# Optimization experiments

Measured on AMD Instinct MI355X. Metric: run time of the kernel, lower is better.

## Reference

```python
import jax, jax.numpy as jnp
import numpy as np

B, D, U = 4096, 256, 512


def setup_inputs() -> dict:
    key = jax.random.key(0)
    k = jax.random.split(key, 7)
    return {
        "x": jax.random.normal(k[0], (B, D), jnp.float32),
        "t": jax.random.uniform(k[1], (B, 1), jnp.float32),           # elapsed-time input
        "h0": jax.random.normal(k[2], (B, U), jnp.float32),
        "c0": jax.random.normal(k[3], (B, U), jnp.float32),
        "kernel": jax.random.normal(k[4], (D, 5 * U), jnp.float32) / np.sqrt(D).astype(np.float32),
        "recurrent_kernel": jax.random.normal(k[5], (U, 3 * U), jnp.float32) / np.sqrt(U).astype(np.float32),
        "kernel_time": jax.random.normal(k[6], (1, 3 * U), jnp.float32) * 0.1,
    }


def reference(x, t, h0, c0, kernel, recurrent_kernel, kernel_time):
    sig = jax.nn.sigmoid
    # Fused input projection: one GEMM instead of 5 (same math, kernel cols are
    # ordered [i, c, o, t1, t2] exactly as the original slices self.kernel).
    x_i, x_c, x_o, x_t1, x_t2 = jnp.split(x @ kernel, 5, axis=1)          # each (B, U)
    # Fused recurrent projection: cols ordered [i, c, o].
    r_i, r_c, r_o = jnp.split(h0 @ recurrent_kernel, 3, axis=1)           # each (B, U)
    # Time projections: cols ordered [t1, t2, o].
    kt1, kt2, kto = jnp.split(t @ kernel_time, 3, axis=1)                 # each (B, U)

    i = sig(x_i + r_i)
    t_1 = sig(x_t1 + sig(kt1))
    # tf.where(t_1 > -1e-5, -1e-5, t_1): sigmoid output is always > -1e-5,
    # so this clamps to the constant -1e-5; keep the where for faithfulness.
    NEG_EPS = jnp.float32(-1e-5)
    t_1_constraint = jnp.where(t_1 > NEG_EPS, jnp.full_like(t_1, NEG_EPS), t_1)
    t_2 = sig(x_t2 + sig(kt2))
    c_tilde = jnp.tanh(x_c + r_c)
    c_m_ = (1.0 - i * t_1) * c0 + i * c_tilde * t_1_constraint
    c_m = (1.0 - i) * c0 + i * c_tilde * t_2
    o = sig(x_o + r_o + kto)
    h = jnp.tanh(c_m_) * o
    # original returns (h, [h, c_m]); h appears twice, so return (h, c_m)
    return (h, c_m)
```

## Files before the change

### kernel.cpp

```cpp
#include <hip/hip_runtime.h>


typedef __attribute__((ext_vector_type(8))) short short8_t;
typedef __attribute__((ext_vector_type(4))) float f32x4_t;
typedef unsigned int u32;

#define B_N 4096
#define D_K 256
#define U_N 512

__device__ __forceinline__ unsigned short f2bf(float f) {
    unsigned int x = __float_as_uint(f);
    unsigned int r = x + 0x7fffu + ((x >> 16) & 1u);
    return (unsigned short)(r >> 16);
}

__device__ __forceinline__ float sigf(float z) {
    return 1.0f / (1.0f + __expf(-z));
}

__device__ __forceinline__ float tanhfast(float z) {
    return 1.0f - 2.0f / (1.0f + __expf(2.0f * z));
}

__device__ __forceinline__ void gl16(const unsigned short* g, unsigned short* l) {
    __builtin_amdgcn_global_load_lds(
        (const __attribute__((address_space(1))) u32*)g,
        (__attribute__((address_space(3))) u32*)l, 16, 0, 0);
}

#define SWZ(r, kc) ((((r) * 8) + ((kc) ^ ((r) & 7))) * 8)

__global__ __launch_bounds__(256) void prep(
    const float* __restrict__ x, const float* __restrict__ h0,
    const float* __restrict__ kern, const float* __restrict__ rk,
    unsigned short* __restrict__ xs, unsigned short* __restrict__ hs,
    unsigned short* __restrict__ ksw, unsigned short* __restrict__ rsw)
{
    const int c = blockIdx.x * 256 + threadIdx.x;
    if (c < 131072) {
        const int t = c >> 10, q = c & 1023;
        const int row = q >> 3, kc = q & 7;
        const int rb = t >> 2, kb = t & 3;
        const float* s = x + (size_t)(rb * 128 + row) * D_K + kb * 64 + kc * 8;
        short8_t o;
#pragma unroll
        for (int j = 0; j < 8; ++j) o[j] = (short)f2bf(s[j]);
        *reinterpret_cast<short8_t*>(xs + (size_t)t * 8192 + SWZ(row, kc)) = o;
    } else if (c < 393216) {
        const int c2 = c - 131072;
        const int t = c2 >> 10, q = c2 & 1023;
        const int row = q >> 3, kc = q & 7;
        const int rb = t >> 3, kb = t & 7;
        const float* s = h0 + (size_t)(rb * 128 + row) * U_N + kb * 64 + kc * 8;
        short8_t o;
#pragma unroll
        for (int j = 0; j < 8; ++j) o[j] = (short)f2bf(s[j]);
        *reinterpret_cast<short8_t*>(hs + (size_t)t * 8192 + SWZ(row, kc)) = o;
    } else if (c < 475136) {
        const int c2 = c - 393216;
        const int t = c2 / 1280, q = c2 - t * 1280;
        const int kc = q / 160, r = q - kc * 160;
        const int nb = t >> 2, kb = t & 3;
        const int col = (r >> 5) * U_N + nb * 32 + (r & 31);
        short8_t o;
#pragma unroll
        for (int j = 0; j < 8; ++j)
            o[j] = (short)f2bf(kern[(size_t)(kb * 64 + kc * 8 + j) * 2560 + col]);
        *reinterpret_cast<short8_t*>(ksw + (size_t)t * 10240 + SWZ(r, kc)) = o;
    } else {
        const int c2 = c - 475136;
        const int t = c2 / 768, q = c2 - t * 768;
        const int kc = q / 96, r = q - kc * 96;
        const int nb = t >> 3, kb = t & 7;
        const int col = (r >> 5) * U_N + nb * 32 + (r & 31);
        short8_t o;
#pragma unroll
        for (int j = 0; j < 8; ++j)
            o[j] = (short)f2bf(rk[(size_t)(kb * 64 + kc * 8 + j) * 1536 + col]);
        *reinterpret_cast<short8_t*>(rsw + (size_t)t * 6144 + SWZ(r, kc)) = o;
    }
}

__global__ __launch_bounds__(256, 2) void tlstm_main(
    const unsigned short* __restrict__ xs,
    const unsigned short* __restrict__ hs,
    const unsigned short* __restrict__ ksw,
    const unsigned short* __restrict__ rsw,
    const float* __restrict__ tvec,
    const float* __restrict__ c0,
    const float* __restrict__ ktime,
    float* __restrict__ out)
{
    __shared__ __align__(16) unsigned short lds[2][18432];

    const int tid = threadIdx.x;
    const int wave = tid >> 6;
    const int lane = tid & 63;
    const int lr = lane & 15;
    const int lq = lane >> 4;
    const int wm = wave >> 1;
    const int wn = wave & 1;
    const int nb = blockIdx.x;
    const int rb = blockIdx.y;

    f32x4_t acc[8][4];
#pragma unroll
    for (int m = 0; m < 8; ++m)
#pragma unroll
        for (int p = 0; p < 4; ++p)
            acc[m][p] = (f32x4_t){0.f, 0.f, 0.f, 0.f};

    auto stage = [&](int s, int buf) {
        unsigned short* ab = &lds[buf][0];
        unsigned short* bb = &lds[buf][8192];
        if (s < 4) {
            const unsigned short* at = xs + (size_t)(rb * 4 + s) * 8192;
#pragma unroll
            for (int j = 0; j < 4; ++j)
                gl16(at + (j * 256 + tid) * 8, ab + (j * 256 + wave * 64) * 8);
            const unsigned short* bt = ksw + (size_t)(nb * 4 + s) * 10240;
#pragma unroll
            for (int j = 0; j < 5; ++j)
                gl16(bt + (j * 256 + tid) * 8, bb + (j * 256 + wave * 64) * 8);
        } else {
            const unsigned short* at = hs + (size_t)(rb * 8 + (s - 4)) * 8192;
#pragma unroll
            for (int j = 0; j < 4; ++j)
                gl16(at + (j * 256 + tid) * 8, ab + (j * 256 + wave * 64) * 8);
            const unsigned short* bt = rsw + (size_t)(nb * 8 + (s - 4)) * 6144;
#pragma unroll
            for (int j = 0; j < 3; ++j)
                gl16(bt + (j * 256 + tid) * 8, bb + (j * 256 + wave * 64) * 8);
        }
    };

    auto compute1 = [&](int buf) {
        const unsigned short* ab = &lds[buf][0];
        const unsigned short* bb = &lds[buf][8192];
#pragma unroll
        for (int ks = 0; ks < 2; ++ks) {
            const int kc = ks * 4 + lq;
            short8_t a[4];
#pragma unroll
            for (int p = 0; p < 4; ++p)
                a[p] = *reinterpret_cast<const short8_t*>(ab + SWZ(wm * 64 + p * 16 + lr, kc));
#pragma unroll
            for (int m = 0; m < 5; ++m) {
                const int r = m * 32 + wn * 16 + lr;
                short8_t b = *reinterpret_cast<const short8_t*>(bb + SWZ(r, kc));
#pragma unroll
                for (int p = 0; p < 4; ++p)
                    acc[m][p] = __builtin_amdgcn_mfma_f32_16x16x32_bf16(a[p], b, acc[m][p], 0, 0, 0);
            }
        }
    };

    auto compute2 = [&](int buf) {
        const unsigned short* ab = &lds[buf][0];
        const unsigned short* bb = &lds[buf][8192];
#pragma unroll
        for (int ks = 0; ks < 2; ++ks) {
            const int kc = ks * 4 + lq;
            short8_t a[4];
#pragma unroll
            for (int p = 0; p < 4; ++p)
                a[p] = *reinterpret_cast<const short8_t*>(ab + SWZ(wm * 64 + p * 16 + lr, kc));
#pragma unroll
            for (int m = 0; m < 3; ++m) {
                const int r = m * 32 + wn * 16 + lr;
                short8_t b = *reinterpret_cast<const short8_t*>(bb + SWZ(r, kc));
#pragma unroll
                for (int p = 0; p < 4; ++p)
                    acc[5 + m][p] = __builtin_amdgcn_mfma_f32_16x16x32_bf16(a[p], b, acc[5 + m][p], 0, 0, 0);
            }
        }
    };

    int cur = 0;
    stage(0, 0);
    __syncthreads();
#pragma unroll 1
    for (int s = 0; s < 12; ++s) {
        if (s < 11) stage(s + 1, cur ^ 1);
        if (s < 4) compute1(cur); else compute2(cur);
        __syncthreads();
        cur ^= 1;
    }

    const float NEG_EPS = -1e-5f;
    const int u = nb * 32 + wn * 16 + lr;
    const float kt1 = ktime[u];
    const float kt2 = ktime[U_N + u];
    const float kto = ktime[2 * U_N + u];
#pragma unroll
    for (int p = 0; p < 4; ++p)
#pragma unroll
        for (int i2 = 0; i2 < 4; ++i2) {
            const int b = rb * 128 + wm * 64 + p * 16 + lq * 4 + i2;
            const float tb = tvec[b];
            const float c0v = c0[(size_t)b * U_N + u];
            const float x_i  = acc[0][p][i2];
            const float x_c  = acc[1][p][i2];
            const float x_o  = acc[2][p][i2];
            const float x_t1 = acc[3][p][i2];
            const float x_t2 = acc[4][p][i2];
            const float r_i  = acc[5][p][i2];
            const float r_c  = acc[6][p][i2];
            const float r_o  = acc[7][p][i2];

            const float ig  = sigf(x_i + r_i);
            const float t1v = sigf(x_t1 + sigf(tb * kt1));
            const float t1c = (t1v > NEG_EPS) ? NEG_EPS : t1v;
            const float t2v = sigf(x_t2 + sigf(tb * kt2));
            const float ct  = tanhfast(x_c + r_c);
            const float cm_ = (1.f - ig * t1v) * c0v + ig * ct * t1c;
            const float cm  = (1.f - ig) * c0v + ig * ct * t2v;
            const float og  = sigf(x_o + r_o + tb * kto);

            out[(size_t)b * U_N + u] = tanhfast(cm_) * og;
            out[(size_t)B_N * U_N + (size_t)b * U_N + u] = cm;
        }

}

extern "C" void kernel_launch(void* const* d_in, const int* in_sizes, int n_in,
                              void* d_out, int out_size, void* d_ws, size_t ws_size,
                              hipStream_t stream) {
    const float* x     = (const float*)d_in[0];
    const float* t     = (const float*)d_in[1];
    const float* h0    = (const float*)d_in[2];
    const float* c0    = (const float*)d_in[3];
    const float* kern  = (const float*)d_in[4];
    const float* rk    = (const float*)d_in[5];
    const float* ktime = (const float*)d_in[6];
    float* out = (float*)d_out;

    unsigned short* xs  = (unsigned short*)d_ws;
    unsigned short* hs  = (unsigned short*)((char*)d_ws + 2097152);
    unsigned short* ksw = (unsigned short*)((char*)d_ws + 6291456);
    unsigned short* rsw = (unsigned short*)((char*)d_ws + 7602176);

    prep<<<2240, 256, 0, stream>>>(x, h0, kern, rk, xs, hs, ksw, rsw);
    tlstm_main<<<dim3(16, 32), 256, 0, stream>>>(
        xs, hs, ksw, rsw, t, c0, ktime, out);
}
```

Baseline: 33.19 us.

## Widen main tile to 64 units with 512 threads and unrolled vmcnt pipeline

Each block now covers 64 hidden units with 8 waves and 512 threads instead of 32 units with 4 waves, so every A tile loaded into LDS serves twice as many columns and the grid halves. The K loop is fully unrolled with explicit s_waitcnt vmcnt and raw barriers in place of __syncthreads, so the next stage's loads can stay in flight while the current stage computes. The c0 values are prefetched into registers during the last stages, hiding their latency before the epilogue. The costs are more LDS per block (about 112 KB for the two buffers), which limits occupancy, and hand-counted vmcnt values that must exactly match the number of loads issued per stage.

```diff
diff --git a/kernel.cpp b/kernel.cpp
--- a/kernel.cpp
+++ b/kernel.cpp
@@ -30,6 +30,10 @@
 }
 
 #define SWZ(r, kc) ((((r) * 8) + ((kc) ^ ((r) & 7))) * 8)
+
+#define WAIT_VM(N)                                            \
+    asm volatile("s_waitcnt vmcnt(" #N ")" ::: "memory");     \
+    __builtin_amdgcn_sched_barrier(0)
 
 __global__ __launch_bounds__(256) void prep(
     const float* __restrict__ x, const float* __restrict__ h0,
@@ -82,7 +86,7 @@
     }
 }
 
-__global__ __launch_bounds__(256, 2) void tlstm_main(
+__global__ __launch_bounds__(512, 2) void tlstm_main(
     const unsigned short* __restrict__ xs,
     const unsigned short* __restrict__ hs,
     const unsigned short* __restrict__ ksw,
@@ -92,46 +96,58 @@
     const float* __restrict__ ktime,
     float* __restrict__ out)
 {
-    __shared__ __align__(16) unsigned short lds[2][18432];
+    __shared__ __align__(16) unsigned short lds[2][28672];
 
     const int tid = threadIdx.x;
     const int wave = tid >> 6;
     const int lane = tid & 63;
     const int lr = lane & 15;
     const int lq = lane >> 4;
-    const int wm = wave >> 1;
-    const int wn = wave & 1;
+    const int wm = wave >> 2;
+    const int wn = wave & 3;
     const int nb = blockIdx.x;
     const int rb = blockIdx.y;
 
+    const int u = nb * 64 + wn * 16 + lr;
+
     f32x4_t acc[8][4];
 #pragma unroll
     for (int m = 0; m < 8; ++m)
 #pragma unroll
         for (int p = 0; p < 4; ++p)
             acc[m][p] = (f32x4_t){0.f, 0.f, 0.f, 0.f};
+
+    float c0r[16];
 
     auto stage = [&](int s, int buf) {
         unsigned short* ab = &lds[buf][0];
         unsigned short* bb = &lds[buf][8192];
         if (s < 4) {
             const unsigned short* at = xs + (size_t)(rb * 4 + s) * 8192;
-#pragma unroll
-            for (int j = 0; j < 4; ++j)
-                gl16(at + (j * 256 + tid) * 8, ab + (j * 256 + wave * 64) * 8);
-            const unsigned short* bt = ksw + (size_t)(nb * 4 + s) * 10240;
-#pragma unroll
-            for (int j = 0; j < 5; ++j)
-                gl16(bt + (j * 256 + tid) * 8, bb + (j * 256 + wave * 64) * 8);
+            gl16(at + (size_t)tid * 8,         ab + (size_t)(wave * 64) * 8);
+            gl16(at + (size_t)(512 + tid) * 8, ab + (size_t)(512 + wave * 64) * 8);
+            const unsigned short* b0 = ksw + (size_t)(nb * 8 + s) * 10240;
+            const unsigned short* b1 = ksw + (size_t)(nb * 8 + 4 + s) * 10240;
+#pragma unroll
+            for (int j = 0; j < 5; ++j) {
+                const int c = j * 512 + tid;
+                const unsigned short* src = (c < 1280) ? (b0 + (size_t)c * 8)
+                                                       : (b1 + (size_t)(c - 1280) * 8);
+                gl16(src, bb + (size_t)(j * 512 + wave * 64) * 8);
+            }
         } else {
             const unsigned short* at = hs + (size_t)(rb * 8 + (s - 4)) * 8192;
-#pragma unroll
-            for (int j = 0; j < 4; ++j)
-                gl16(at + (j * 256 + tid) * 8, ab + (j * 256 + wave * 64) * 8);
-            const unsigned short* bt = rsw + (size_t)(nb * 8 + (s - 4)) * 6144;
-#pragma unroll
-            for (int j = 0; j < 3; ++j)
-                gl16(bt + (j * 256 + tid) * 8, bb + (j * 256 + wave * 64) * 8);
+            gl16(at + (size_t)tid * 8,         ab + (size_t)(wave * 64) * 8);
+            gl16(at + (size_t)(512 + tid) * 8, ab + (size_t)(512 + wave * 64) * 8);
+            const unsigned short* b0 = rsw + (size_t)(nb * 16 + (s - 4)) * 6144;
+            const unsigned short* b1 = rsw + (size_t)(nb * 16 + 8 + (s - 4)) * 6144;
+#pragma unroll
+            for (int j = 0; j < 3; ++j) {
+                const int c = j * 512 + tid;
+                const unsigned short* src = (c < 768) ? (b0 + (size_t)c * 8)
+                                                      : (b1 + (size_t)(c - 768) * 8);
+                gl16(src, bb + (size_t)(j * 512 + wave * 64) * 8);
+            }
         }
     };
 
@@ -147,7 +163,7 @@
                 a[p] = *reinterpret_cast<const short8_t*>(ab + SWZ(wm * 64 + p * 16 + lr, kc));
 #pragma unroll
             for (int m = 0; m < 5; ++m) {
-                const int r = m * 32 + wn * 16 + lr;
+                const int r = (wn >> 1) * 160 + m * 32 + (wn & 1) * 16 + lr;
                 short8_t b = *reinterpret_cast<const short8_t*>(bb + SWZ(r, kc));
 #pragma unroll
                 for (int p = 0; p < 4; ++p)
@@ -168,7 +184,7 @@
                 a[p] = *reinterpret_cast<const short8_t*>(ab + SWZ(wm * 64 + p * 16 + lr, kc));
 #pragma unroll
             for (int m = 0; m < 3; ++m) {
-                const int r = m * 32 + wn * 16 + lr;
+                const int r = (wn >> 1) * 96 + m * 32 + (wn & 1) * 16 + lr;
                 short8_t b = *reinterpret_cast<const short8_t*>(bb + SWZ(r, kc));
 #pragma unroll
                 for (int p = 0; p < 4; ++p)
@@ -177,19 +193,41 @@
         }
     };
 
-    int cur = 0;
+#define K_BODY(S, NV, CF)                                  \
+    {                                                      \
+        WAIT_VM(NV);                                       \
+        __builtin_amdgcn_s_barrier();                      \
+        __builtin_amdgcn_sched_barrier(0);                 \
+        CF((S) & 1);                                       \
+        __builtin_amdgcn_sched_barrier(0);                 \
+        __builtin_amdgcn_s_barrier();                      \
+        __builtin_amdgcn_sched_barrier(0);                 \
+    }
+
     stage(0, 0);
-    __syncthreads();
-#pragma unroll 1
-    for (int s = 0; s < 12; ++s) {
-        if (s < 11) stage(s + 1, cur ^ 1);
-        if (s < 4) compute1(cur); else compute2(cur);
-        __syncthreads();
-        cur ^= 1;
-    }
+    stage(1, 1);  K_BODY(0, 7,  compute1);
+    stage(2, 0);  K_BODY(1, 7,  compute1);
+    stage(3, 1);  K_BODY(2, 7,  compute1);
+    stage(4, 0);  K_BODY(3, 5,  compute1);
+    stage(5, 1);  K_BODY(4, 5,  compute2);
+    stage(6, 0);  K_BODY(5, 5,  compute2);
+    stage(7, 1);  K_BODY(6, 5,  compute2);
+    stage(8, 0);  K_BODY(7, 5,  compute2);
+    stage(9, 1);
+    asm volatile("" ::: "memory");
+#pragma unroll
+    for (int p = 0; p < 4; ++p)
+#pragma unroll
+        for (int i2 = 0; i2 < 4; ++i2) {
+            const int b = rb * 128 + wm * 64 + p * 16 + lq * 4 + i2;
+            c0r[p * 4 + i2] = c0[(size_t)b * U_N + u];
+        }
+    K_BODY(8, 21, compute2);
+    stage(10, 0); K_BODY(9, 21, compute2);
+    stage(11, 1); K_BODY(10, 5, compute2);
+    K_BODY(11, 0, compute2);
 
     const float NEG_EPS = -1e-5f;
-    const int u = nb * 32 + wn * 16 + lr;
     const float kt1 = ktime[u];
     const float kt2 = ktime[U_N + u];
     const float kto = ktime[2 * U_N + u];
@@ -199,7 +237,7 @@
         for (int i2 = 0; i2 < 4; ++i2) {
             const int b = rb * 128 + wm * 64 + p * 16 + lq * 4 + i2;
             const float tb = tvec[b];
-            const float c0v = c0[(size_t)b * U_N + u];
+            const float c0v = c0r[p * 4 + i2];
             const float x_i  = acc[0][p][i2];
             const float x_c  = acc[1][p][i2];
             const float x_o  = acc[2][p][i2];
@@ -221,7 +259,6 @@
             out[(size_t)b * U_N + u] = tanhfast(cm_) * og;
             out[(size_t)B_N * U_N + (size_t)b * U_N + u] = cm;
         }
-
 }
 
 extern "C" void kernel_launch(void* const* d_in, const int* in_sizes, int n_in,
@@ -242,6 +279,6 @@
     unsigned short* rsw = (unsigned short*)((char*)d_ws + 7602176);
 
     prep<<<2240, 256, 0, stream>>>(x, h0, kern, rk, xs, hs, ksw, rsw);
-    tlstm_main<<<dim3(16, 32), 256, 0, stream>>>(
+    tlstm_main<<<dim3(8, 32), 512, 0, stream>>>(
         xs, hs, ksw, rsw, t, c0, ktime, out);
 }
```

Result: slower. 35.80 us (+7.9%).

## Fully unroll K loop with explicit vmcnt waits for async LDS prefetch

Applied to the files above, without the earlier changes.

Replaces the rolled double-buffered loop, which used __syncthreads after each step, with a fully unrolled sequence. Each step issues the next stage's global-to-LDS loads, then waits only on the previous stage's loads using a counted s_waitcnt vmcnt, with raw barriers and sched_barriers around the compute. This lets the prefetch of stage s+1 stay in flight while stage s computes, where before a full drain forced a wait. It depends on hand-counted vmcnt values matching the per-stage load counts; a wrong count could read stale LDS data.

```diff
diff --git a/kernel.cpp b/kernel.cpp
--- a/kernel.cpp
+++ b/kernel.cpp
@@ -30,6 +30,10 @@
 }
 
 #define SWZ(r, kc) ((((r) * 8) + ((kc) ^ ((r) & 7))) * 8)
+
+#define WAIT_VM(N)                                            \
+    asm volatile("s_waitcnt vmcnt(" #N ")" ::: "memory");     \
+    __builtin_amdgcn_sched_barrier(0)
 
 __global__ __launch_bounds__(256) void prep(
     const float* __restrict__ x, const float* __restrict__ h0,
@@ -177,16 +181,30 @@
         }
     };
 
-    int cur = 0;
+#define K_BODY(S, NV, CF)                                  \
+    {                                                      \
+        WAIT_VM(NV);                                       \
+        __builtin_amdgcn_s_barrier();                      \
+        __builtin_amdgcn_sched_barrier(0);                 \
+        CF((S) & 1);                                       \
+        __builtin_amdgcn_sched_barrier(0);                 \
+        __builtin_amdgcn_s_barrier();                      \
+        __builtin_amdgcn_sched_barrier(0);                 \
+    }
+
     stage(0, 0);
-    __syncthreads();
-#pragma unroll 1
-    for (int s = 0; s < 12; ++s) {
-        if (s < 11) stage(s + 1, cur ^ 1);
-        if (s < 4) compute1(cur); else compute2(cur);
-        __syncthreads();
-        cur ^= 1;
-    }
+    stage(1, 1);   K_BODY(0, 9, compute1);
+    stage(2, 0);   K_BODY(1, 9, compute1);
+    stage(3, 1);   K_BODY(2, 9, compute1);
+    stage(4, 0);   K_BODY(3, 7, compute1);
+    stage(5, 1);   K_BODY(4, 7, compute2);
+    stage(6, 0);   K_BODY(5, 7, compute2);
+    stage(7, 1);   K_BODY(6, 7, compute2);
+    stage(8, 0);   K_BODY(7, 7, compute2);
+    stage(9, 1);   K_BODY(8, 7, compute2);
+    stage(10, 0);  K_BODY(9, 7, compute2);
+    stage(11, 1);  K_BODY(10, 7, compute2);
+    K_BODY(11, 0, compute2);
 
     const float NEG_EPS = -1e-5f;
     const int u = nb * 32 + wn * 16 + lr;
@@ -221,7 +239,6 @@
             out[(size_t)b * U_N + u] = tanhfast(cm_) * og;
             out[(size_t)B_N * U_N + (size_t)b * U_N + u] = cm;
         }
-
 }
 
 extern "C" void kernel_launch(void* const* d_in, const int* in_sizes, int n_in,
```

New measurement: 32.73 us. No clear change (-1.4%).

## Fuse fp32-to-bf16 conversion of x and h0 into GEMM A-tile loads

Applied to the files above, without the earlier changes.

The prep kernel no longer converts and swizzles x and h0 into bf16 workspace buffers. The main kernel now loads fp32 A tiles into registers, issues those loads before the MFMA compute of the current stage, and converts and writes them to LDS afterwards. This removes a full write and re-read of the converted activations plus most of the prep launch work. The cost is that each of the 16 column blocks re-reads and re-converts the fp32 activations, with more register pressure and VALU work in the main loop. The t1 clamp is also folded to the constant NEG_EPS.

```diff
diff --git a/kernel.cpp b/kernel.cpp
--- a/kernel.cpp
+++ b/kernel.cpp
@@ -32,34 +32,12 @@
 #define SWZ(r, kc) ((((r) * 8) + ((kc) ^ ((r) & 7))) * 8)
 
 __global__ __launch_bounds__(256) void prep(
-    const float* __restrict__ x, const float* __restrict__ h0,
     const float* __restrict__ kern, const float* __restrict__ rk,
-    unsigned short* __restrict__ xs, unsigned short* __restrict__ hs,
     unsigned short* __restrict__ ksw, unsigned short* __restrict__ rsw)
 {
     const int c = blockIdx.x * 256 + threadIdx.x;
-    if (c < 131072) {
-        const int t = c >> 10, q = c & 1023;
-        const int row = q >> 3, kc = q & 7;
-        const int rb = t >> 2, kb = t & 3;
-        const float* s = x + (size_t)(rb * 128 + row) * D_K + kb * 64 + kc * 8;
-        short8_t o;
-#pragma unroll
-        for (int j = 0; j < 8; ++j) o[j] = (short)f2bf(s[j]);
-        *reinterpret_cast<short8_t*>(xs + (size_t)t * 8192 + SWZ(row, kc)) = o;
-    } else if (c < 393216) {
-        const int c2 = c - 131072;
-        const int t = c2 >> 10, q = c2 & 1023;
-        const int row = q >> 3, kc = q & 7;
-        const int rb = t >> 3, kb = t & 7;
-        const float* s = h0 + (size_t)(rb * 128 + row) * U_N + kb * 64 + kc * 8;
-        short8_t o;
-#pragma unroll
-        for (int j = 0; j < 8; ++j) o[j] = (short)f2bf(s[j]);
-        *reinterpret_cast<short8_t*>(hs + (size_t)t * 8192 + SWZ(row, kc)) = o;
-    } else if (c < 475136) {
-        const int c2 = c - 393216;
-        const int t = c2 / 1280, q = c2 - t * 1280;
+    if (c < 81920) {
+        const int t = c / 1280, q = c - t * 1280;
         const int kc = q / 160, r = q - kc * 160;
         const int nb = t >> 2, kb = t & 3;
         const int col = (r >> 5) * U_N + nb * 32 + (r & 31);
@@ -69,7 +47,7 @@
             o[j] = (short)f2bf(kern[(size_t)(kb * 64 + kc * 8 + j) * 2560 + col]);
         *reinterpret_cast<short8_t*>(ksw + (size_t)t * 10240 + SWZ(r, kc)) = o;
     } else {
-        const int c2 = c - 475136;
+        const int c2 = c - 81920;
         const int t = c2 / 768, q = c2 - t * 768;
         const int kc = q / 96, r = q - kc * 96;
         const int nb = t >> 3, kb = t & 7;
@@ -83,8 +61,8 @@
 }
 
 __global__ __launch_bounds__(256, 2) void tlstm_main(
-    const unsigned short* __restrict__ xs,
-    const unsigned short* __restrict__ hs,
+    const float* __restrict__ x,
+    const float* __restrict__ h0,
     const unsigned short* __restrict__ ksw,
     const unsigned short* __restrict__ rsw,
     const float* __restrict__ tvec,
@@ -111,23 +89,45 @@
         for (int p = 0; p < 4; ++p)
             acc[m][p] = (f32x4_t){0.f, 0.f, 0.f, 0.f};
 
-    auto stage = [&](int s, int buf) {
+    f32x4_t va[4][2];
+
+    auto loadA = [&](int s) {
+        const float* base;
+        int ld, kb;
+        if (s < 4) { base = x  + (size_t)rb * 128 * D_K; ld = D_K; kb = s; }
+        else       { base = h0 + (size_t)rb * 128 * U_N; ld = U_N; kb = s - 4; }
+#pragma unroll
+        for (int j = 0; j < 4; ++j) {
+            const int c = j * 256 + tid, row = c >> 3, kc = c & 7;
+            const float* p = base + (size_t)row * ld + kb * 64 + kc * 8;
+            va[j][0] = *reinterpret_cast<const f32x4_t*>(p);
+            va[j][1] = *reinterpret_cast<const f32x4_t*>(p + 4);
+        }
+    };
+
+    auto writeA = [&](int buf) {
         unsigned short* ab = &lds[buf][0];
+#pragma unroll
+        for (int j = 0; j < 4; ++j) {
+            const int c = j * 256 + tid, row = c >> 3, kc = c & 7;
+            short8_t o;
+#pragma unroll
+            for (int e = 0; e < 4; ++e) {
+                o[e]     = (short)f2bf(va[j][0][e]);
+                o[4 + e] = (short)f2bf(va[j][1][e]);
+            }
+            *reinterpret_cast<short8_t*>(ab + SWZ(row, kc)) = o;
+        }
+    };
+
+    auto stageB = [&](int s, int buf) {
         unsigned short* bb = &lds[buf][8192];
         if (s < 4) {
-            const unsigned short* at = xs + (size_t)(rb * 4 + s) * 8192;
-#pragma unroll
-            for (int j = 0; j < 4; ++j)
-                gl16(at + (j * 256 + tid) * 8, ab + (j * 256 + wave * 64) * 8);
             const unsigned short* bt = ksw + (size_t)(nb * 4 + s) * 10240;
 #pragma unroll
             for (int j = 0; j < 5; ++j)
                 gl16(bt + (j * 256 + tid) * 8, bb + (j * 256 + wave * 64) * 8);
         } else {
-            const unsigned short* at = hs + (size_t)(rb * 8 + (s - 4)) * 8192;
-#pragma unroll
-            for (int j = 0; j < 4; ++j)
-                gl16(at + (j * 256 + tid) * 8, ab + (j * 256 + wave * 64) * 8);
             const unsigned short* bt = rsw + (size_t)(nb * 8 + (s - 4)) * 6144;
 #pragma unroll
             for (int j = 0; j < 3; ++j)
@@ -177,13 +177,14 @@
         }
     };
 
+    loadA(0); stageB(0, 0); writeA(0);
+    __syncthreads();
     int cur = 0;
-    stage(0, 0);
-    __syncthreads();
 #pragma unroll 1
     for (int s = 0; s < 12; ++s) {
-        if (s < 11) stage(s + 1, cur ^ 1);
+        if (s < 11) { loadA(s + 1); stageB(s + 1, cur ^ 1); }
         if (s < 4) compute1(cur); else compute2(cur);
+        if (s < 11) writeA(cur ^ 1);
         __syncthreads();
         cur ^= 1;
     }
@@ -211,17 +212,15 @@
 
             const float ig  = sigf(x_i + r_i);
             const float t1v = sigf(x_t1 + sigf(tb * kt1));
-            const float t1c = (t1v > NEG_EPS) ? NEG_EPS : t1v;
             const float t2v = sigf(x_t2 + sigf(tb * kt2));
             const float ct  = tanhfast(x_c + r_c);
-            const float cm_ = (1.f - ig * t1v) * c0v + ig * ct * t1c;
+            const float cm_ = (1.f - ig * t1v) * c0v + ig * ct * NEG_EPS;
             const float cm  = (1.f - ig) * c0v + ig * ct * t2v;
             const float og  = sigf(x_o + r_o + tb * kto);
 
             out[(size_t)b * U_N + u] = tanhfast(cm_) * og;
             out[(size_t)B_N * U_N + (size_t)b * U_N + u] = cm;
         }
-
 }
 
 extern "C" void kernel_launch(void* const* d_in, const int* in_sizes, int n_in,
@@ -236,12 +235,10 @@
     const float* ktime = (const float*)d_in[6];
     float* out = (float*)d_out;
 
-    unsigned short* xs  = (unsigned short*)d_ws;
-    unsigned short* hs  = (unsigned short*)((char*)d_ws + 2097152);
     unsigned short* ksw = (unsigned short*)((char*)d_ws + 6291456);
     unsigned short* rsw = (unsigned short*)((char*)d_ws + 7602176);
 
-    prep<<<2240, 256, 0, stream>>>(x, h0, kern, rk, xs, hs, ksw, rsw);
+    prep<<<704, 256, 0, stream>>>(kern, rk, ksw, rsw);
     tlstm_main<<<dim3(16, 32), 256, 0, stream>>>(
-        xs, hs, ksw, rsw, t, c0, ktime, out);
-}
+        x, h0, ksw, rsw, t, c0, ktime, out);
+}
```

Result: slower. 67.58 us (+103.6%).
